# Kernel optimization log

Measured on AMD Instinct MI355X. Metric: run time of the kernel, lower is better.

The kernel has to match this reference:

```python
import jax, jax.numpy as jnp
import numpy as np
import math

E = 1024      # embed_dim
H = 16        # num_heads
DK = E // H   # k_dim per head
DV = E // H   # v_dim per head
T = 2048      # tgt_len
S = 2048      # src_len
B = 2         # batch
SCALING = DK ** -0.5
D_THRESH = math.log(2000.0 / 40.0 - 1.0)  # epoch defaults to 40 -> log(49)


def setup_inputs() -> dict:
    key = jax.random.key(0)
    ks = jax.random.split(key, 8)
    inp = {
        "query": jax.random.normal(ks[0], (T, B, E), jnp.float32),
        "key": jax.random.normal(ks[1], (S, B, E), jnp.float32),
        "value": jax.random.normal(ks[2], (S, B, E), jnp.float32),
        "mask": jnp.ones((T, S), jnp.int32),
        # projection params (torch Linear: y = x @ W.T + b)
        "Wq": jax.random.normal(ks[3], (H * DK, E), jnp.float32) * 0.02,
        "bq": jnp.zeros((H * DK,), jnp.float32),
        "Wk": jax.random.normal(ks[4], (H * DK, E), jnp.float32) * 0.02,
        "bk": jnp.zeros((H * DK,), jnp.float32),
        "Wv": jax.random.normal(ks[5], (H * DV, E), jnp.float32) * 0.02,
        "bv": jnp.zeros((H * DV,), jnp.float32),
        "Wo": jax.random.normal(ks[6], (E, H * DV), jnp.float32) * 0.02,
        "bo": jnp.zeros((E,), jnp.float32),
    }
    return inp


def reference(query, key, value, mask, Wq, bq, Wk, bk, Wv, bv, Wo, bo):
    bsz, tgt_len, src_len = query.shape[1], query.shape[0], value.shape[0]
    q = (jnp.einsum('tbe,fe->tbf', query, Wq) + bq) * SCALING
    k = jnp.einsum('sbe,fe->sbf', key, Wk) + bk
    v = jnp.einsum('sbe,fe->sbf', value, Wv) + bv
    # [T, B, H*d] -> [B*H, T, d]  (same memory split as torch .view)
    q = q.reshape(tgt_len, bsz * H, DK).transpose(1, 0, 2)
    k = k.reshape(src_len, bsz * H, DK).transpose(1, 0, 2)
    v = v.reshape(src_len, bsz * H, DV).transpose(1, 0, 2)
    attn_weights = jnp.einsum('ztd,zsd->zts', q, k)  # [B*H, T, S]
    neg_inf = jnp.float32(-jnp.inf)
    attn_weights = jnp.where(mask[None, :, :] == 0, neg_inf, attn_weights)
    # eval-mode dynamic threshold mask (no Gumbel/exponential noise)
    aw_max = jnp.max(attn_weights, axis=-1, keepdims=True)
    drop = attn_weights < (aw_max - D_THRESH)
    attn_weights = jnp.where(drop, neg_inf, attn_weights)
    attn_weights = jax.nn.softmax(attn_weights, axis=-1)
    attn = jnp.einsum('zts,zsd->ztd', attn_weights, v)  # [B*H, T, DV]
    attn = attn.transpose(1, 0, 2).reshape(tgt_len, bsz, H * DV)
    attn = jnp.einsum('tbf,ef->tbe', attn, Wo) + bo
    return attn, attn_weights
```

## Files before the change

### kernel.cpp

```cpp
#include <hip/hip_runtime.h>
#include <hip/hip_bf16.h>
#include <math.h>

#define TT 2048
#define SS 2048
#define BB 2
#define EE 1024
#define HH 16
#define DD 64
#define ZZ 32
#define QSCALE 0.18033688011112042f
#define D_THRESH2 5.6147098441152083f

#define LDP 72

typedef unsigned short ushort_t;
typedef __attribute__((ext_vector_type(8))) short bf16x8;
typedef __attribute__((ext_vector_type(4))) float f32x4;

__device__ __forceinline__ float fexp2(float x) { return __builtin_amdgcn_exp2f(x); }

__device__ __forceinline__ ushort_t f2bf(float f) {
    unsigned u = __float_as_uint(f);
    return (ushort_t)((u + 0x7fffu + ((u >> 16) & 1u)) >> 16);
}

__device__ __forceinline__ void cvt8r(const float4 x, const float4 y, ushort_t* __restrict__ dst) {
    union { __hip_bfloat162 h[4]; bf16x8 v; } t;
    t.h[0] = __float22bfloat162_rn(make_float2(x.x, x.y));
    t.h[1] = __float22bfloat162_rn(make_float2(x.z, x.w));
    t.h[2] = __float22bfloat162_rn(make_float2(y.x, y.y));
    t.h[3] = __float22bfloat162_rn(make_float2(y.z, y.w));
    *(bf16x8*)dst = t.v;
}

__global__ __launch_bounds__(256) void maskpack_kernel(const int* __restrict__ mask,
                                                       unsigned long long* __restrict__ mb)
{
    const int gw = (blockIdx.x * 256 + threadIdx.x) >> 6;
    const int lane = threadIdx.x & 63;
    for (int i = 0; i < 16; ++i) {
        const size_t w64 = (size_t)gw * 16 + i;
        const int v = mask[w64 * 64 + lane];
        const unsigned long long b = __ballot(v != 0);
        if (lane == 0) mb[w64] = b;
    }
}

__global__ __launch_bounds__(256) void projb_kernel(const float* __restrict__ X,
                                                    const float* __restrict__ W,
                                                    const float* __restrict__ bias,
                                                    ushort_t* __restrict__ out,
                                                    float scale)
{
    __shared__ __align__(16) ushort_t Al[2][128 * LDP];
    __shared__ __align__(16) ushort_t Bl[2][64 * LDP];
    const int tid = threadIdx.x;
    const int lane = tid & 63, wid = tid >> 6;
    const int ln = lane & 15, quad = lane >> 4;
    const int R0 = blockIdx.x * 128, C0 = blockIdx.y * 64;
    const int rA = tid >> 1, cA = (tid & 1) * 32;
    const int rB = tid >> 2, cB = (tid & 3) * 16;

    const float* sa = X + (size_t)(R0 + rA) * EE + cA;
    const float* sb = W + (size_t)(C0 + rB) * EE + cB;

    float4 pa[8], pb[4];
#pragma unroll
    for (int j = 0; j < 8; ++j) pa[j] = *(const float4*)(sa + j * 4);
#pragma unroll
    for (int j = 0; j < 4; ++j) pb[j] = *(const float4*)(sb + j * 4);

    f32x4 acc[2][4] = {};
    for (int kc = 0; kc < 16; ++kc) {
        const int buf = kc & 1;
        {
            ushort_t* da = &Al[buf][rA * LDP + cA];
            cvt8r(pa[0], pa[1], da);
            cvt8r(pa[2], pa[3], da + 8);
            cvt8r(pa[4], pa[5], da + 16);
            cvt8r(pa[6], pa[7], da + 24);
            ushort_t* db = &Bl[buf][rB * LDP + cB];
            cvt8r(pb[0], pb[1], db);
            cvt8r(pb[2], pb[3], db + 8);
        }
        __syncthreads();
        if (kc < 15) {
            sa += 64; sb += 64;
#pragma unroll
            for (int j = 0; j < 8; ++j) pa[j] = *(const float4*)(sa + j * 4);
#pragma unroll
            for (int j = 0; j < 4; ++j) pb[j] = *(const float4*)(sb + j * 4);
        }
#pragma unroll
        for (int ks = 0; ks < 2; ++ks) {
            bf16x8 af[2], bfr[4];
#pragma unroll
            for (int i = 0; i < 2; ++i)
                af[i] = *(const bf16x8*)&Al[buf][(wid * 32 + i * 16 + ln) * LDP + ks * 32 + quad * 8];
#pragma unroll
            for (int j = 0; j < 4; ++j)
                bfr[j] = *(const bf16x8*)&Bl[buf][(j * 16 + ln) * LDP + ks * 32 + quad * 8];
#pragma unroll
            for (int rt = 0; rt < 2; ++rt)
#pragma unroll
                for (int ct = 0; ct < 4; ++ct)
                    acc[rt][ct] = __builtin_amdgcn_mfma_f32_16x16x32_bf16(
                        af[rt], bfr[ct], acc[rt][ct], 0, 0, 0);
        }
    }
#pragma unroll
    for (int ct = 0; ct < 4; ++ct) {
        const int f = C0 + ct * 16 + ln;
        const float bv = bias[f];
        const int h = f >> 6, d = f & 63;
#pragma unroll
        for (int rt = 0; rt < 2; ++rt)
#pragma unroll
            for (int reg = 0; reg < 4; ++reg) {
                const int R = R0 + wid * 32 + rt * 16 + quad * 4 + reg;
                const int t = R >> 1, b = R & 1;
                const float v = (acc[rt][ct][reg] + bv) * scale;
                out[((size_t)((b << 4) + h) * TT + t) * DD + d] = f2bf(v);
            }
    }
}

__global__ __launch_bounds__(256) void vtrans_kernel(const ushort_t* __restrict__ vb,
                                                     ushort_t* __restrict__ vtb)
{
    __shared__ __align__(16) ushort_t tsh[64][LDP];
    const int tid = threadIdx.x;
    const int z = blockIdx.y, s0 = blockIdx.x * 64;
    const int r = tid >> 2, g = (tid & 3) * 16;
    const ushort_t* src = vb + ((size_t)z * SS + s0 + r) * DD + g;
    *(bf16x8*)&tsh[r][g]     = *(const bf16x8*)src;
    *(bf16x8*)&tsh[r][g + 8] = *(const bf16x8*)(src + 8);
    __syncthreads();
    const int d = tid >> 2;
    union { ushort_t u[16]; } t;
#pragma unroll
    for (int j = 0; j < 16; ++j) t.u[j] = tsh[g + j][d];
    ushort_t* dst = vtb + ((size_t)z * DD + d) * SS + s0 + g;
    *(bf16x8*)dst       = *(bf16x8*)&t.u[0];
    *(bf16x8*)(dst + 8) = *(bf16x8*)&t.u[8];
}

__global__ __launch_bounds__(256) void attnb_kernel(const ushort_t* __restrict__ qb,
                                                    const ushort_t* __restrict__ kb,
                                                    const ushort_t* __restrict__ vtb,
                                                    const unsigned long long* __restrict__ mb,
                                                    float* __restrict__ out1,
                                                    ushort_t* __restrict__ avb)
{
    __shared__ __align__(16) ushort_t Ks[64 * LDP];
    __shared__ __align__(16) ushort_t Vts[64 * LDP];
    __shared__ __align__(16) ushort_t Pl[4][16 * LDP];
    __shared__ unsigned long long Ml[64];
    const int tid = threadIdx.x;
    const int lane = tid & 63, wid = tid >> 6;
    const int ln = lane & 15, quad = lane >> 4;
    const int rr = quad * 4;
    const int z = blockIdx.y, t0 = blockIdx.x * 64;
    const int srL = tid >> 2, sgr = (tid & 3) * 16;

    const ushort_t* qrow = qb + ((size_t)z * TT + t0 + wid * 16 + ln) * DD;
    const bf16x8 aq0 = *(const bf16x8*)(qrow + quad * 8);
    const bf16x8 aq1 = *(const bf16x8*)(qrow + 32 + quad * 8);

    const ushort_t* kbase = kb + ((size_t)z * SS + srL) * DD + sgr;
    const ushort_t* vbase = vtb + ((size_t)z * DD + srL) * SS + sgr;
    const unsigned long long* mrow = mb + (size_t)(t0 + (tid & 63)) * 32;

    float mx[4] = {-1e30f, -1e30f, -1e30f, -1e30f};
    float zl[4] = {0.f, 0.f, 0.f, 0.f};

    bf16x8 pk0 = *(const bf16x8*)kbase;
    bf16x8 pk1 = *(const bf16x8*)(kbase + 8);
    unsigned long long pml = (tid < 64) ? mrow[0] : 0ULL;
    for (int st = 0; st < 32; ++st) {
        __syncthreads();
        *(bf16x8*)&Ks[srL * LDP + sgr]     = pk0;
        *(bf16x8*)&Ks[srL * LDP + sgr + 8] = pk1;
        if (tid < 64) Ml[tid] = pml;
        __syncthreads();
        if (st < 31) {
            const ushort_t* src = kbase + (size_t)(st + 1) * 64 * DD;
            pk0 = *(const bf16x8*)src;
            pk1 = *(const bf16x8*)(src + 8);
            if (tid < 64) pml = mrow[st + 1];
        }
        const bool allfull = __all(Ml[wid * 16 + ln] == ~0ULL);
        unsigned long long wm[4];
        if (!allfull) {
#pragma unroll
            for (int reg = 0; reg < 4; ++reg) wm[reg] = Ml[wid * 16 + rr + reg];
        }
#pragma unroll
        for (int nt = 0; nt < 4; ++nt) {
            const ushort_t* kp = &Ks[(nt * 16 + ln) * LDP + quad * 8];
            const bf16x8 b0 = *(const bf16x8*)kp;
            const bf16x8 b1 = *(const bf16x8*)(kp + 32);
            f32x4 lg = {};
            lg = __builtin_amdgcn_mfma_f32_16x16x32_bf16(aq0, b0, lg, 0, 0, 0);
            lg = __builtin_amdgcn_mfma_f32_16x16x32_bf16(aq1, b1, lg, 0, 0, 0);
            if (allfull) {
#pragma unroll
                for (int reg = 0; reg < 4; ++reg) {
                    zl[reg] += fexp2(lg[reg]);
                    mx[reg] = fmaxf(mx[reg], lg[reg]);
                }
            } else {
#pragma unroll
                for (int reg = 0; reg < 4; ++reg) {
                    const bool keep = (wm[reg] >> (nt * 16 + ln)) & 1ULL;
                    const float l = keep ? lg[reg] : -2e30f;
                    zl[reg] += fexp2(l);
                    mx[reg] = fmaxf(mx[reg], l);
                }
            }
        }
    }
#pragma unroll
    for (int off = 1; off < 16; off <<= 1) {
#pragma unroll
        for (int reg = 0; reg < 4; ++reg) {
            zl[reg] += __shfl_xor(zl[reg], off, 64);
            mx[reg] = fmaxf(mx[reg], __shfl_xor(mx[reg], off, 64));
        }
    }
    float rz[4], thr[4];
#pragma unroll
    for (int reg = 0; reg < 4; ++reg) {
        rz[reg]  = 1.f / zl[reg];
        thr[reg] = mx[reg] - D_THRESH2;
    }

    f32x4 o[4] = {};
    pk0 = *(const bf16x8*)kbase;
    pk1 = *(const bf16x8*)(kbase + 8);
    bf16x8 pv0 = *(const bf16x8*)vbase;
    bf16x8 pv1 = *(const bf16x8*)(vbase + 8);
    pml = (tid < 64) ? mrow[0] : 0ULL;
    float* o1w = out1 + ((size_t)z * TT + t0 + wid * 16) * SS;
    ushort_t* plw = &Pl[wid][0];
    for (int st = 0; st < 32; ++st) {
        __syncthreads();
        *(bf16x8*)&Ks[srL * LDP + sgr]      = pk0;
        *(bf16x8*)&Ks[srL * LDP + sgr + 8]  = pk1;
        *(bf16x8*)&Vts[srL * LDP + sgr]     = pv0;
        *(bf16x8*)&Vts[srL * LDP + sgr + 8] = pv1;
        if (tid < 64) Ml[tid] = pml;
        __syncthreads();
        if (st < 31) {
            const ushort_t* ksrc = kbase + (size_t)(st + 1) * 64 * DD;
            pk0 = *(const bf16x8*)ksrc;
            pk1 = *(const bf16x8*)(ksrc + 8);
            const ushort_t* vsrc = vbase + (st + 1) * 64;
            pv0 = *(const bf16x8*)vsrc;
            pv1 = *(const bf16x8*)(vsrc + 8);
            if (tid < 64) pml = mrow[st + 1];
        }
        const bool allfull = __all(Ml[wid * 16 + ln] == ~0ULL);
        unsigned long long wm[4];
        if (!allfull) {
#pragma unroll
            for (int reg = 0; reg < 4; ++reg) wm[reg] = Ml[wid * 16 + rr + reg];
        }
        float* o1st = o1w + st * 64;
#pragma unroll
        for (int nt = 0; nt < 4; ++nt) {
            const ushort_t* kp = &Ks[(nt * 16 + ln) * LDP + quad * 8];
            const bf16x8 b0 = *(const bf16x8*)kp;
            const bf16x8 b1 = *(const bf16x8*)(kp + 32);
            f32x4 lg = {};
            lg = __builtin_amdgcn_mfma_f32_16x16x32_bf16(aq0, b0, lg, 0, 0, 0);
            lg = __builtin_amdgcn_mfma_f32_16x16x32_bf16(aq1, b1, lg, 0, 0, 0);
#pragma unroll
            for (int reg = 0; reg < 4; ++reg) {
                float l = lg[reg];
                if (!allfull && !((wm[reg] >> (nt * 16 + ln)) & 1ULL)) l = -2e30f;
                const float e = fexp2(l) * rz[reg];
                const float wv = (l >= thr[reg]) ? e : 0.f;
                o1st[(size_t)(rr + reg) * SS + nt * 16 + ln] = wv;
                plw[(rr + reg) * LDP + nt * 16 + ln] = f2bf(wv);
            }
        }
#pragma unroll
        for (int ks = 0; ks < 2; ++ks) {
            const bf16x8 ap = *(const bf16x8*)&plw[ln * LDP + ks * 32 + quad * 8];
#pragma unroll
            for (int dt = 0; dt < 4; ++dt) {
                const bf16x8 bv = *(const bf16x8*)&Vts[(dt * 16 + ln) * LDP + ks * 32 + quad * 8];
                o[dt] = __builtin_amdgcn_mfma_f32_16x16x32_bf16(ap, bv, o[dt], 0, 0, 0);
            }
        }
    }
#pragma unroll
    for (int dt = 0; dt < 4; ++dt)
#pragma unroll
        for (int reg = 0; reg < 4; ++reg)
            avb[((size_t)z * TT + t0 + wid * 16 + rr + reg) * DD + dt * 16 + ln] =
                f2bf(o[dt][reg]);
}

__global__ __launch_bounds__(256) void oprojb_kernel(const ushort_t* __restrict__ avb,
                                                     const float* __restrict__ Wo,
                                                     const float* __restrict__ bo,
                                                     float* __restrict__ out0)
{
    __shared__ __align__(16) ushort_t Al[2][128 * LDP];
    __shared__ __align__(16) ushort_t Bl[2][64 * LDP];
    const int tid = threadIdx.x;
    const int lane = tid & 63, wid = tid >> 6;
    const int ln = lane & 15, quad = lane >> 4;
    const int R0 = blockIdx.x * 128, C0 = blockIdx.y * 64;
    const int rA = tid >> 1, cA = (tid & 1) * 32;
    const int rB = tid >> 2, cB = (tid & 3) * 16;
    const int tA = (R0 + rA) >> 1, bA = (R0 + rA) & 1;

    const ushort_t* sa = avb + ((size_t)(bA << 4) * TT + tA) * DD + cA;
    const float* sb = Wo + (size_t)(C0 + rB) * EE + cB;

    bf16x8 pa[4];
    float4 pb[4];
#pragma unroll
    for (int j = 0; j < 4; ++j) pa[j] = *(const bf16x8*)(sa + j * 8);
#pragma unroll
    for (int j = 0; j < 4; ++j) pb[j] = *(const float4*)(sb + j * 4);

    f32x4 acc[2][4] = {};
    for (int kc = 0; kc < 16; ++kc) {
        const int buf = kc & 1;
        {
            ushort_t* da = &Al[buf][rA * LDP + cA];
#pragma unroll
            for (int j = 0; j < 4; ++j) *(bf16x8*)(da + j * 8) = pa[j];
            ushort_t* db = &Bl[buf][rB * LDP + cB];
            cvt8r(pb[0], pb[1], db);
            cvt8r(pb[2], pb[3], db + 8);
        }
        __syncthreads();
        if (kc < 15) {
            sa += (size_t)TT * DD;
            sb += 64;
#pragma unroll
            for (int j = 0; j < 4; ++j) pa[j] = *(const bf16x8*)(sa + j * 8);
#pragma unroll
            for (int j = 0; j < 4; ++j) pb[j] = *(const float4*)(sb + j * 4);
        }
#pragma unroll
        for (int ks = 0; ks < 2; ++ks) {
            bf16x8 af[2], bfr[4];
#pragma unroll
            for (int i = 0; i < 2; ++i)
                af[i] = *(const bf16x8*)&Al[buf][(wid * 32 + i * 16 + ln) * LDP + ks * 32 + quad * 8];
#pragma unroll
            for (int j = 0; j < 4; ++j)
                bfr[j] = *(const bf16x8*)&Bl[buf][(j * 16 + ln) * LDP + ks * 32 + quad * 8];
#pragma unroll
            for (int rt = 0; rt < 2; ++rt)
#pragma unroll
                for (int ct = 0; ct < 4; ++ct)
                    acc[rt][ct] = __builtin_amdgcn_mfma_f32_16x16x32_bf16(
                        af[rt], bfr[ct], acc[rt][ct], 0, 0, 0);
        }
    }
#pragma unroll
    for (int ct = 0; ct < 4; ++ct) {
        const int e = C0 + ct * 16 + ln;
        const float bv = bo[e];
#pragma unroll
        for (int rt = 0; rt < 2; ++rt)
#pragma unroll
            for (int reg = 0; reg < 4; ++reg) {
                const int R = R0 + wid * 32 + rt * 16 + quad * 4 + reg;
                out0[(size_t)R * EE + e] = acc[rt][ct][reg] + bv;
            }
    }
}


extern "C" void kernel_launch(void* const* d_in, const int* in_sizes, int n_in,
                              void* d_out, int out_size, void* d_ws, size_t ws_size,
                              hipStream_t stream)
{
    const float* query = (const float*)d_in[0];
    const float* key   = (const float*)d_in[1];
    const float* value = (const float*)d_in[2];
    const int*   mask  = (const int*)d_in[3];
    const float* Wq = (const float*)d_in[4];
    const float* bq = (const float*)d_in[5];
    const float* Wk = (const float*)d_in[6];
    const float* bk = (const float*)d_in[7];
    const float* Wv = (const float*)d_in[8];
    const float* bv = (const float*)d_in[9];
    const float* Wo = (const float*)d_in[10];
    const float* bo = (const float*)d_in[11];

    float* out0 = (float*)d_out;
    float* out1 = out0 + (size_t)TT * BB * EE;

    char* ws = (char*)d_ws;
    const size_t nzd = (size_t)ZZ * TT * DD;
    ushort_t* qb  = (ushort_t*)ws;
    ushort_t* kb  = qb + nzd;
    ushort_t* vb  = kb + nzd;
    ushort_t* vtb = vb + nzd;
    ushort_t* avb = vtb + nzd;
    unsigned long long* mb = (unsigned long long*)(avb + nzd);

    const dim3 blk(256);

    maskpack_kernel<<<dim3(1024), blk, 0, stream>>>(mask, mb);

    const dim3 gproj(TT * BB / 128, EE / 64);
    projb_kernel<<<gproj, blk, 0, stream>>>(query, Wq, bq, qb, QSCALE);
    projb_kernel<<<gproj, blk, 0, stream>>>(key,   Wk, bk, kb, 1.0f);
    projb_kernel<<<gproj, blk, 0, stream>>>(value, Wv, bv, vb, 1.0f);

    vtrans_kernel<<<dim3(SS / 64, ZZ), blk, 0, stream>>>(vb, vtb);

    attnb_kernel<<<dim3(TT / 64, ZZ), blk, 0, stream>>>(qb, kb, vtb, mb, out1, avb);

    oprojb_kernel<<<gproj, blk, 0, stream>>>(avb, Wo, bo, out0);
}
```

Baseline: 930.7 us.

## Transpose QK MFMA so each lane owns one query row, vectorize stores

Swaps the MFMA operand order so the logits tile is transposed: each lane holds four consecutive key columns of a single query row. This lets each lane keep one running max/sum instead of four, shrinks the cross-lane reduction to two shuffles, and has each lane load its own mask word instead of staging masks through shared memory with an extra barrier. The attention-weight output and the bf16 P tile are now written as float4 and packed bf16x4 stores rather than scalar scatters. Every lane now issues its own global mask load, and the P tile layout in shared memory changes, which could introduce bank conflicts.

Result: faster. 906.8 us (-2.6%).

```diff
diff --git a/kernel.cpp b/kernel.cpp
--- a/kernel.cpp
+++ b/kernel.cpp
@@ -16,6 +16,7 @@
 
 typedef unsigned short ushort_t;
 typedef __attribute__((ext_vector_type(8))) short bf16x8;
+typedef __attribute__((ext_vector_type(4))) short bf16x4;
 typedef __attribute__((ext_vector_type(4))) float f32x4;
 
 __device__ __forceinline__ float fexp2(float x) { return __builtin_amdgcn_exp2f(x); }
@@ -32,6 +33,13 @@
     t.h[2] = __float22bfloat162_rn(make_float2(y.x, y.y));
     t.h[3] = __float22bfloat162_rn(make_float2(y.z, y.w));
     *(bf16x8*)dst = t.v;
+}
+
+__device__ __forceinline__ bf16x4 pack4(float a, float b, float c, float d) {
+    union { __hip_bfloat162 h[2]; bf16x4 v; } t;
+    t.h[0] = __float22bfloat162_rn(make_float2(a, b));
+    t.h[1] = __float22bfloat162_rn(make_float2(c, d));
+    return t.v;
 }
 
 __global__ __launch_bounds__(256) void maskpack_kernel(const int* __restrict__ mask,
@@ -156,7 +164,6 @@
     __shared__ __align__(16) ushort_t Ks[64 * LDP];
     __shared__ __align__(16) ushort_t Vts[64 * LDP];
     __shared__ __align__(16) ushort_t Pl[4][16 * LDP];
-    __shared__ unsigned long long Ml[64];
     const int tid = threadIdx.x;
     const int lane = tid & 63, wid = tid >> 6;
     const int ln = lane & 15, quad = lane >> 4;
@@ -165,84 +172,68 @@
     const int srL = tid >> 2, sgr = (tid & 3) * 16;
 
     const ushort_t* qrow = qb + ((size_t)z * TT + t0 + wid * 16 + ln) * DD;
-    const bf16x8 aq0 = *(const bf16x8*)(qrow + quad * 8);
-    const bf16x8 aq1 = *(const bf16x8*)(qrow + 32 + quad * 8);
+    const bf16x8 bq0 = *(const bf16x8*)(qrow + quad * 8);
+    const bf16x8 bq1 = *(const bf16x8*)(qrow + 32 + quad * 8);
 
     const ushort_t* kbase = kb + ((size_t)z * SS + srL) * DD + sgr;
     const ushort_t* vbase = vtb + ((size_t)z * DD + srL) * SS + sgr;
-    const unsigned long long* mrow = mb + (size_t)(t0 + (tid & 63)) * 32;
-
-    float mx[4] = {-1e30f, -1e30f, -1e30f, -1e30f};
-    float zl[4] = {0.f, 0.f, 0.f, 0.f};
+    const unsigned long long* mrow = mb + (size_t)(t0 + wid * 16 + ln) * 32;
+
+    float mx = -1e30f, zl = 0.f;
 
     bf16x8 pk0 = *(const bf16x8*)kbase;
     bf16x8 pk1 = *(const bf16x8*)(kbase + 8);
-    unsigned long long pml = (tid < 64) ? mrow[0] : 0ULL;
+    unsigned long long pml = mrow[0];
     for (int st = 0; st < 32; ++st) {
         __syncthreads();
         *(bf16x8*)&Ks[srL * LDP + sgr]     = pk0;
         *(bf16x8*)&Ks[srL * LDP + sgr + 8] = pk1;
-        if (tid < 64) Ml[tid] = pml;
-        __syncthreads();
+        __syncthreads();
+        const unsigned long long w = pml;
         if (st < 31) {
             const ushort_t* src = kbase + (size_t)(st + 1) * 64 * DD;
             pk0 = *(const bf16x8*)src;
             pk1 = *(const bf16x8*)(src + 8);
-            if (tid < 64) pml = mrow[st + 1];
-        }
-        const bool allfull = __all(Ml[wid * 16 + ln] == ~0ULL);
-        unsigned long long wm[4];
-        if (!allfull) {
-#pragma unroll
-            for (int reg = 0; reg < 4; ++reg) wm[reg] = Ml[wid * 16 + rr + reg];
-        }
+            pml = mrow[st + 1];
+        }
+        const bool allfull = __all(w == ~0ULL);
 #pragma unroll
         for (int nt = 0; nt < 4; ++nt) {
             const ushort_t* kp = &Ks[(nt * 16 + ln) * LDP + quad * 8];
-            const bf16x8 b0 = *(const bf16x8*)kp;
-            const bf16x8 b1 = *(const bf16x8*)(kp + 32);
+            const bf16x8 a0 = *(const bf16x8*)kp;
+            const bf16x8 a1 = *(const bf16x8*)(kp + 32);
             f32x4 lg = {};
-            lg = __builtin_amdgcn_mfma_f32_16x16x32_bf16(aq0, b0, lg, 0, 0, 0);
-            lg = __builtin_amdgcn_mfma_f32_16x16x32_bf16(aq1, b1, lg, 0, 0, 0);
+            lg = __builtin_amdgcn_mfma_f32_16x16x32_bf16(a0, bq0, lg, 0, 0, 0);
+            lg = __builtin_amdgcn_mfma_f32_16x16x32_bf16(a1, bq1, lg, 0, 0, 0);
             if (allfull) {
+                zl += (fexp2(lg[0]) + fexp2(lg[1])) + (fexp2(lg[2]) + fexp2(lg[3]));
+                mx = fmaxf(mx, fmaxf(fmaxf(lg[0], lg[1]), fmaxf(lg[2], lg[3])));
+            } else {
+                const int base = nt * 16 + rr;
 #pragma unroll
                 for (int reg = 0; reg < 4; ++reg) {
-                    zl[reg] += fexp2(lg[reg]);
-                    mx[reg] = fmaxf(mx[reg], lg[reg]);
-                }
-            } else {
-#pragma unroll
-                for (int reg = 0; reg < 4; ++reg) {
-                    const bool keep = (wm[reg] >> (nt * 16 + ln)) & 1ULL;
+                    const bool keep = (w >> (base + reg)) & 1ULL;
                     const float l = keep ? lg[reg] : -2e30f;
-                    zl[reg] += fexp2(l);
-                    mx[reg] = fmaxf(mx[reg], l);
+                    zl += fexp2(l);
+                    mx = fmaxf(mx, l);
                 }
             }
         }
     }
-#pragma unroll
-    for (int off = 1; off < 16; off <<= 1) {
-#pragma unroll
-        for (int reg = 0; reg < 4; ++reg) {
-            zl[reg] += __shfl_xor(zl[reg], off, 64);
-            mx[reg] = fmaxf(mx[reg], __shfl_xor(mx[reg], off, 64));
-        }
-    }
-    float rz[4], thr[4];
-#pragma unroll
-    for (int reg = 0; reg < 4; ++reg) {
-        rz[reg]  = 1.f / zl[reg];
-        thr[reg] = mx[reg] - D_THRESH2;
-    }
+    zl += __shfl_xor(zl, 16, 64);
+    mx = fmaxf(mx, __shfl_xor(mx, 16, 64));
+    zl += __shfl_xor(zl, 32, 64);
+    mx = fmaxf(mx, __shfl_xor(mx, 32, 64));
+    const float rz  = 1.f / zl;
+    const float thr = mx - D_THRESH2;
 
     f32x4 o[4] = {};
     pk0 = *(const bf16x8*)kbase;
     pk1 = *(const bf16x8*)(kbase + 8);
     bf16x8 pv0 = *(const bf16x8*)vbase;
     bf16x8 pv1 = *(const bf16x8*)(vbase + 8);
-    pml = (tid < 64) ? mrow[0] : 0ULL;
-    float* o1w = out1 + ((size_t)z * TT + t0 + wid * 16) * SS;
+    pml = mrow[0];
+    float* o1p = out1 + ((size_t)z * TT + t0 + wid * 16 + ln) * SS;
     ushort_t* plw = &Pl[wid][0];
     for (int st = 0; st < 32; ++st) {
         __syncthreads();
@@ -250,8 +241,8 @@
         *(bf16x8*)&Ks[srL * LDP + sgr + 8]  = pk1;
         *(bf16x8*)&Vts[srL * LDP + sgr]     = pv0;
         *(bf16x8*)&Vts[srL * LDP + sgr + 8] = pv1;
-        if (tid < 64) Ml[tid] = pml;
-        __syncthreads();
+        __syncthreads();
+        const unsigned long long w = pml;
         if (st < 31) {
             const ushort_t* ksrc = kbase + (size_t)(st + 1) * 64 * DD;
             pk0 = *(const bf16x8*)ksrc;
@@ -259,32 +250,30 @@
             const ushort_t* vsrc = vbase + (st + 1) * 64;
             pv0 = *(const bf16x8*)vsrc;
             pv1 = *(const bf16x8*)(vsrc + 8);
-            if (tid < 64) pml = mrow[st + 1];
-        }
-        const bool allfull = __all(Ml[wid * 16 + ln] == ~0ULL);
-        unsigned long long wm[4];
-        if (!allfull) {
-#pragma unroll
-            for (int reg = 0; reg < 4; ++reg) wm[reg] = Ml[wid * 16 + rr + reg];
-        }
-        float* o1st = o1w + st * 64;
+            pml = mrow[st + 1];
+        }
+        const bool allfull = __all(w == ~0ULL);
+        float* o1st = o1p + st * 64;
 #pragma unroll
         for (int nt = 0; nt < 4; ++nt) {
             const ushort_t* kp = &Ks[(nt * 16 + ln) * LDP + quad * 8];
-            const bf16x8 b0 = *(const bf16x8*)kp;
-            const bf16x8 b1 = *(const bf16x8*)(kp + 32);
+            const bf16x8 a0 = *(const bf16x8*)kp;
+            const bf16x8 a1 = *(const bf16x8*)(kp + 32);
             f32x4 lg = {};
-            lg = __builtin_amdgcn_mfma_f32_16x16x32_bf16(aq0, b0, lg, 0, 0, 0);
-            lg = __builtin_amdgcn_mfma_f32_16x16x32_bf16(aq1, b1, lg, 0, 0, 0);
+            lg = __builtin_amdgcn_mfma_f32_16x16x32_bf16(a0, bq0, lg, 0, 0, 0);
+            lg = __builtin_amdgcn_mfma_f32_16x16x32_bf16(a1, bq1, lg, 0, 0, 0);
+            const int base = nt * 16 + rr;
+            float wv[4];
 #pragma unroll
             for (int reg = 0; reg < 4; ++reg) {
                 float l = lg[reg];
-                if (!allfull && !((wm[reg] >> (nt * 16 + ln)) & 1ULL)) l = -2e30f;
-                const float e = fexp2(l) * rz[reg];
-                const float wv = (l >= thr[reg]) ? e : 0.f;
-                o1st[(size_t)(rr + reg) * SS + nt * 16 + ln] = wv;
-                plw[(rr + reg) * LDP + nt * 16 + ln] = f2bf(wv);
+                if (!allfull && !((w >> (base + reg)) & 1ULL)) l = -2e30f;
+                const float e = fexp2(l) * rz;
+                wv[reg] = (l >= thr) ? e : 0.f;
             }
+            float4 o4; o4.x = wv[0]; o4.y = wv[1]; o4.z = wv[2]; o4.w = wv[3];
+            *(float4*)(o1st + base) = o4;
+            *(bf16x4*)&plw[ln * LDP + base] = pack4(wv[0], wv[1], wv[2], wv[3]);
         }
 #pragma unroll
         for (int ks = 0; ks < 2; ++ks) {
```
